# Performance work log

Measured on AMD Instinct MI355X. Metric: run time of the kernel, lower is better.

Reference implementation:

```python
import jax, jax.numpy as jnp
import numpy as np

B, S, D = 2, 1024, 1024
H, KVH, HD = 16, 4, 64  # query heads, kv heads, head_dim
EPS = 1e-5
SCALE = float(np.sqrt(HD))  # note: scale uses original head_dim, not concat dim


def rmsnorm(x, g):
    return x * jax.lax.rsqrt(jnp.mean(x * x, axis=-1, keepdims=True) + EPS) * g


def rope(x, cos, sin):
    # x: [B,S,h,HD]; cos/sin: [S, HD//2]; pairs are consecutive (view_as_complex layout)
    xr = x.reshape(*x.shape[:-1], HD // 2, 2)
    x0, x1 = xr[..., 0], xr[..., 1]
    c = cos[None, :, None, :]
    s = sin[None, :, None, :]
    o0 = x0 * c - x1 * s
    o1 = x0 * s + x1 * c
    return jnp.stack([o0, o1], axis=-1).reshape(x.shape)


def context_build(x, W, gq, gk):
    comb = x @ W.T  # [B,S, H*HD + 2*KVH*HD]
    q, k, v = jnp.split(comb, [H * HD, H * HD + KVH * HD], axis=-1)
    q = rmsnorm(q, gq).reshape(B, S, H, HD)
    k = rmsnorm(k, gk).reshape(B, S, KVH, HD)
    v = v.reshape(B, S, KVH, HD)
    return q, k, v


def setup_inputs() -> dict:
    key = jax.random.key(0)
    ks = jax.random.split(key, 12)
    total = H * HD + 2 * KVH * HD  # 1536
    pos = jnp.arange(S, dtype=jnp.float32)
    theta = 10000.0 ** (-jnp.arange(0, HD, 2, dtype=jnp.float32) / HD)  # [HD//2]
    ang = pos[:, None] * theta[None, :]  # [S, HD//2]
    sc = 0.02
    return {
        "local_c": jax.random.normal(ks[0], (B, S, D), jnp.float32),
        "global_c": jax.random.normal(ks[1], (B, S, D), jnp.float32),
        "freqs_cos": jnp.cos(ang),
        "freqs_sin": jnp.sin(ang),
        "W_lc": jax.random.normal(ks[2], (total, D), jnp.float32) * sc,
        "W_gc": jax.random.normal(ks[3], (total, D), jnp.float32) * sc,
        "g_q_lc": jnp.ones((H * HD,), jnp.float32),
        "g_k_lc": jnp.ones((KVH * HD,), jnp.float32),
        "g_q_gc": jnp.ones((H * HD,), jnp.float32),
        "g_k_gc": jnp.ones((KVH * HD,), jnp.float32),
        "W_local": jax.random.normal(ks[4], (H * HD, 2 * H * HD), jnp.float32) * sc,
        "b_local": jnp.zeros((H * HD,), jnp.float32),
        "g_lc_out": jnp.ones((H * HD,), jnp.float32),
        "W_global": jax.random.normal(ks[5], (H * HD, 2 * H * HD), jnp.float32) * sc,
        "b_global": jnp.zeros((H * HD,), jnp.float32),
        "g_gc_out": jnp.ones((H * HD,), jnp.float32),
    }


def reference(local_c, global_c, freqs_cos, freqs_sin, W_lc, W_gc,
              g_q_lc, g_k_lc, g_q_gc, g_k_gc,
              W_local, b_local, g_lc_out, W_global, b_global, g_gc_out):
    q_lc, k_lc, v_lc = context_build(local_c, W_lc, g_q_lc, g_k_lc)
    q_gc, k_gc, v_gc = context_build(global_c, W_gc, g_q_gc, g_k_gc)

    q_lc = rope(q_lc, freqs_cos, freqs_sin)
    k_lc = rope(k_lc, freqs_cos, freqs_sin)
    q_gc = rope(q_gc, freqs_cos, freqs_sin)
    k_gc = rope(k_gc, freqs_cos, freqs_sin)

    # concat local+global along head_dim -> per-head dim 2*HD
    q = jnp.concatenate([q_lc, q_gc], axis=-1)  # [B,S,H,2HD]
    k = jnp.concatenate([k_lc, k_gc], axis=-1)  # [B,S,KVH,2HD]
    v = jnp.concatenate([v_lc, v_gc], axis=-1)

    n_rep = H // KVH
    k = jnp.repeat(k, n_rep, axis=2)  # [B,S,H,2HD] (GQA repeat_kv)
    v = jnp.repeat(v, n_rep, axis=2)

    scores = jnp.einsum("bqhd,bkhd->bhqk", q, k) / SCALE  # [B,H,S,S]
    attn = jax.nn.softmax(scores, axis=-1)
    out = jnp.einsum("bhqk,bkhd->bqhd", attn, v).reshape(B, S, H * 2 * HD)

    x_lc = rmsnorm(out @ W_local.T + b_local, g_lc_out)
    x_gc = rmsnorm(out @ W_global.T + b_global, g_gc_out)
    return (x_lc, x_gc)
```

## Files before the change

kernel.cpp:

```cpp
#include <hip/hip_runtime.h>

typedef __attribute__((ext_vector_type(8))) __bf16 bf16x8;
typedef __attribute__((ext_vector_type(4))) __bf16 bf16x4;
typedef __attribute__((ext_vector_type(4))) float f32x4;

__device__ __forceinline__ bf16x8 cvt8(const float* __restrict__ p)
{
    const float4 a = *(const float4*)p;
    const float4 b = *(const float4*)(p + 4);
    bf16x8 r;
    r[0] = (__bf16)a.x; r[1] = (__bf16)a.y; r[2] = (__bf16)a.z; r[3] = (__bf16)a.w;
    r[4] = (__bf16)b.x; r[5] = (__bf16)b.y; r[6] = (__bf16)b.z; r[7] = (__bf16)b.w;
    return r;
}

__device__ __forceinline__ void gld16(const __bf16* g, __bf16* l)
{
    __builtin_amdgcn_global_load_lds(
        (const __attribute__((address_space(1))) void*)g,
        (__attribute__((address_space(3))) void*)l, 16, 0, 0);
}

struct CvtArgs {
    const float* s[6];
    __bf16* d[6];
    int n[6];
};

__global__ __launch_bounds__(256) void cvt_bf16(CvtArgs a)
{
    const int t = blockIdx.y;
    const int i0 = (blockIdx.x * 256 + threadIdx.x) * 8;
    if (i0 < a.n[t])
        *(bf16x8*)(a.d[t] + i0) = cvt8(a.s[t] + i0);
}

template <typename CT>
__device__ __forceinline__ void gemm_core(const __bf16* __restrict__ Ap, int lda,
                                          const __bf16* __restrict__ Bp, int ldb,
                                          CT* __restrict__ Cp, int ldc, int K)
{
    __shared__ __bf16 As[128 * 32];
    __shared__ __bf16 Bs[128 * 32];
    const int tid  = threadIdx.x;
    const int w    = tid >> 6;
    const int lane = tid & 63;
    const int ln   = lane & 15;
    const int quad = lane >> 4;
    const int wm   = w & 1;
    const int wn   = w >> 1;

    const int srow = 32 * w + (lane >> 2);
    const int scol = (lane & 3) * 8;

    f32x4 acc[4][4];
    const f32x4 zero = {0.f, 0.f, 0.f, 0.f};
#pragma unroll
    for (int i = 0; i < 4; i++)
#pragma unroll
        for (int j = 0; j < 4; j++) acc[i][j] = zero;

    for (int k0 = 0; k0 < K; k0 += 32) {
        __syncthreads();
        gld16(Ap + (size_t)srow * lda        + k0 + scol, As + (2 * w)     * 512 + lane * 8);
        gld16(Ap + (size_t)(srow + 16) * lda + k0 + scol, As + (2 * w + 1) * 512 + lane * 8);
        gld16(Bp + (size_t)srow * ldb        + k0 + scol, Bs + (2 * w)     * 512 + lane * 8);
        gld16(Bp + (size_t)(srow + 16) * ldb + k0 + scol, Bs + (2 * w + 1) * 512 + lane * 8);
        __syncthreads();

        bf16x8 af[4], bw[4];
#pragma unroll
        for (int i = 0; i < 4; i++)
            af[i] = *(const bf16x8*)(As + (wm * 64 + i * 16 + ln) * 32 + quad * 8);
#pragma unroll
        for (int j = 0; j < 4; j++)
            bw[j] = *(const bf16x8*)(Bs + (wn * 64 + j * 16 + ln) * 32 + quad * 8);
#pragma unroll
        for (int i = 0; i < 4; i++)
#pragma unroll
            for (int j = 0; j < 4; j++)
                acc[i][j] = __builtin_amdgcn_mfma_f32_16x16x32_bf16(
                    af[i], bw[j], acc[i][j], 0, 0, 0);
    }

#pragma unroll
    for (int i = 0; i < 4; i++)
#pragma unroll
        for (int j = 0; j < 4; j++)
#pragma unroll
            for (int r = 0; r < 4; r++) {
                const int ml = wm * 64 + i * 16 + quad * 4 + r;
                const int nl = wn * 64 + j * 16 + ln;
                Cp[(size_t)ml * ldc + nl] = (CT)acc[i][j][r];
            }
}

__global__ __launch_bounds__(256) void gemm_qkv(const __bf16* __restrict__ Xbf,
                                                const __bf16* __restrict__ Wqkv,
                                                __bf16* __restrict__ comb)
{
    const int z = blockIdx.z;
    const __bf16* A = Xbf  + (size_t)z * 2048 * 1024 + (size_t)blockIdx.y * 128 * 1024;
    const __bf16* B = Wqkv + (size_t)z * 1536 * 1024 + (size_t)blockIdx.x * 128 * 1024;
    __bf16* C = comb + (size_t)z * 2048 * 1536 +
                (size_t)blockIdx.y * 128 * 1536 + (size_t)blockIdx.x * 128;
    gemm_core<__bf16>(A, 1024, B, 1024, C, 1536, 1024);
}

__global__ __launch_bounds__(256) void gemm_out(const __bf16* __restrict__ AO,
                                                const __bf16* __restrict__ Wout,
                                                float* __restrict__ Y0,
                                                float* __restrict__ Y1)
{
    const int kh = blockIdx.z;
    const __bf16* A = AO   + (size_t)blockIdx.y * 128 * 2048 + kh * 1024;
    const __bf16* B = Wout + (size_t)blockIdx.x * 128 * 2048 + kh * 1024;
    float* Y = kh ? Y1 : Y0;
    float* C = Y + (size_t)blockIdx.y * 128 * 2048 + (size_t)blockIdx.x * 128;
    gemm_core<float>(A, 2048, B, 2048, C, 2048, 1024);
}

__global__ __launch_bounds__(256) void pack_qkv(
    const __bf16* __restrict__ comb,
    const float* __restrict__ fcos, const float* __restrict__ fsin,
    const float* __restrict__ g_q_lc, const float* __restrict__ g_k_lc,
    const float* __restrict__ g_q_gc, const float* __restrict__ g_k_gc,
    __bf16* __restrict__ Qb, __bf16* __restrict__ Kb, __bf16* __restrict__ Vtb)
{
    const int m = blockIdx.x, ctx = blockIdx.y;
    const int b = m >> 10, s = m & 1023;
    const int tid = threadIdx.x;
    const __bf16* cr = comb + ((size_t)ctx * 2048 + m) * 1536;
    const float* gq = ctx ? g_q_gc : g_q_lc;
    const float* gk = ctx ? g_k_gc : g_k_lc;

    const bf16x4 qv = *(const bf16x4*)(cr + tid * 4);
    float sq = (float)qv[0] * (float)qv[0] + (float)qv[1] * (float)qv[1] +
               (float)qv[2] * (float)qv[2] + (float)qv[3] * (float)qv[3];
    const float kvv = (float)cr[1024 + tid];
    float sk = kvv * kvv;
#pragma unroll
    for (int off = 32; off > 0; off >>= 1) {
        sq += __shfl_down(sq, off);
        sk += __shfl_down(sk, off);
    }
    __shared__ float redq[4], redk[4];
    if ((tid & 63) == 0) { redq[tid >> 6] = sq; redk[tid >> 6] = sk; }
    __syncthreads();
    sq = redq[0] + redq[1] + redq[2] + redq[3];
    sk = redk[0] + redk[1] + redk[2] + redk[3];
    const float rq = rsqrtf(sq * (1.f / 1024.f) + 1e-5f);
    const float rk = rsqrtf(sk * (1.f / 256.f) + 1e-5f);

#pragma unroll
    for (int pp = 0; pp < 2; pp++) {
        const int p = tid + pp * 256;
        const int h = p >> 5, pi = p & 31;
        const float x0 = (float)cr[2 * p]     * rq * gq[2 * p];
        const float x1 = (float)cr[2 * p + 1] * rq * gq[2 * p + 1];
        const float c  = fcos[s * 32 + pi];
        const float sn = fsin[s * 32 + pi];
        const float o0 = x0 * c - x1 * sn;
        const float o1 = x0 * sn + x1 * c;
        const size_t qo = ((size_t)m * 16 + h) * 128 + ctx * 64 + 2 * pi;
        Qb[qo]     = (__bf16)o0;
        Qb[qo + 1] = (__bf16)o1;
    }
    if (tid < 128) {
        const int p = tid;
        const int kvh = p >> 5, pi = p & 31;
        const float x0 = (float)cr[1024 + 2 * p]     * rk * gk[2 * p];
        const float x1 = (float)cr[1024 + 2 * p + 1] * rk * gk[2 * p + 1];
        const float c  = fcos[s * 32 + pi];
        const float sn = fsin[s * 32 + pi];
        const float o0 = x0 * c - x1 * sn;
        const float o1 = x0 * sn + x1 * c;
        const size_t ko = ((size_t)(b * 4 + kvh) * 1024 + s) * 128 + ctx * 64 + 2 * pi;
        Kb[ko]     = (__bf16)o0;
        Kb[ko + 1] = (__bf16)o1;
    }
    {
        const int kvh = tid >> 6, d = tid & 63;
        Vtb[((size_t)(b * 4 + kvh) * 128 + ctx * 64 + d) * 1024 + s] = cr[1280 + tid];
    }
}

__global__ __launch_bounds__(256) void attn(const __bf16* __restrict__ Qb,
                                            const __bf16* __restrict__ Kb,
                                            const __bf16* __restrict__ Vtb,
                                            __bf16* __restrict__ AO)
{
    __shared__ __bf16 Ks[64][136];
    __shared__ __bf16 Vts[128][72];
    __shared__ __bf16 Ps[4][16][72];

    const int tid  = threadIdx.x;
    const int w    = tid >> 6;
    const int lane = tid & 63;
    const int ln   = lane & 15;
    const int quad = lane >> 4;
    const int qt = blockIdx.x, h = blockIdx.y, b = blockIdx.z;
    const int kv = h >> 2;

    const __bf16* Kbase = Kb  + (size_t)(b * 4 + kv) * 1024 * 128;
    const __bf16* Vbase = Vtb + (size_t)(b * 4 + kv) * 128 * 1024;

    bf16x8 qf[4];
    const int qrow = qt * 64 + w * 16 + ln;
    const __bf16* qptr = Qb + ((size_t)(b * 1024 + qrow) * 16 + h) * 128;
#pragma unroll
    for (int kc = 0; kc < 4; kc++)
        qf[kc] = *(const bf16x8*)(qptr + kc * 32 + quad * 8);

    f32x4 oacc[8];
    const f32x4 zero = {0.f, 0.f, 0.f, 0.f};
#pragma unroll
    for (int j = 0; j < 8; j++) oacc[j] = zero;
    float mrow[4], lrow[4];
#pragma unroll
    for (int r = 0; r < 4; r++) { mrow[r] = -1e30f; lrow[r] = 0.f; }

    for (int kt = 0; kt < 16; kt++) {
        __syncthreads();
        const int ks0 = kt * 64;
#pragma unroll
        for (int c = tid; c < 1024; c += 256) {
            const int row = c >> 4, seg = c & 15;
            *(bf16x8*)&Ks[row][seg * 8] =
                *(const bf16x8*)(Kbase + (size_t)(ks0 + row) * 128 + seg * 8);
        }
#pragma unroll
        for (int c = tid; c < 1024; c += 256) {
            const int row = c >> 3, seg = c & 7;
            *(bf16x8*)&Vts[row][seg * 8] =
                *(const bf16x8*)(Vbase + (size_t)row * 1024 + ks0 + seg * 8);
        }
        __syncthreads();

        f32x4 sacc[4];
#pragma unroll
        for (int j = 0; j < 4; j++) {
            f32x4 a = zero;
#pragma unroll
            for (int kc = 0; kc < 4; kc++) {
                const bf16x8 kf =
                    *(const bf16x8*)&Ks[j * 16 + ln][kc * 32 + quad * 8];
                a = __builtin_amdgcn_mfma_f32_16x16x32_bf16(qf[kc], kf, a, 0, 0, 0);
            }
            sacc[j] = a * 0.125f;
        }

        float alpha_[4], pexp[4][4];
#pragma unroll
        for (int r = 0; r < 4; r++) {
            float mx = fmaxf(fmaxf(sacc[0][r], sacc[1][r]),
                             fmaxf(sacc[2][r], sacc[3][r]));
#pragma unroll
            for (int off = 1; off < 16; off <<= 1)
                mx = fmaxf(mx, __shfl_xor(mx, off));
            const float mn = fmaxf(mrow[r], mx);
            alpha_[r] = __expf(mrow[r] - mn);
            mrow[r] = mn;
            float rs = 0.f;
#pragma unroll
            for (int j = 0; j < 4; j++) {
                const float p = __expf(sacc[j][r] - mn);
                pexp[j][r] = p;
                rs += p;
            }
#pragma unroll
            for (int off = 1; off < 16; off <<= 1)
                rs += __shfl_xor(rs, off);
            lrow[r] = lrow[r] * alpha_[r] + rs;
        }
#pragma unroll
        for (int j2 = 0; j2 < 8; j2++) {
            f32x4 o = oacc[j2];
#pragma unroll
            for (int r = 0; r < 4; r++) o[r] *= alpha_[r];
            oacc[j2] = o;
        }
#pragma unroll
        for (int j = 0; j < 4; j++)
#pragma unroll
            for (int r = 0; r < 4; r++)
                Ps[w][quad * 4 + r][j * 16 + ln] = (__bf16)pexp[j][r];
        __syncthreads();
#pragma unroll
        for (int kk = 0; kk < 2; kk++) {
            const bf16x8 pf = *(const bf16x8*)&Ps[w][ln][kk * 32 + quad * 8];
#pragma unroll
            for (int j2 = 0; j2 < 8; j2++) {
                const bf16x8 vf =
                    *(const bf16x8*)&Vts[j2 * 16 + ln][kk * 32 + quad * 8];
                oacc[j2] = __builtin_amdgcn_mfma_f32_16x16x32_bf16(pf, vf, oacc[j2], 0, 0, 0);
            }
        }
    }

    float inv[4];
#pragma unroll
    for (int r = 0; r < 4; r++) inv[r] = 1.f / lrow[r];
#pragma unroll
    for (int j2 = 0; j2 < 8; j2++)
#pragma unroll
        for (int r = 0; r < 4; r++) {
            const size_t row = (size_t)(b * 1024 + qt * 64 + w * 16 + quad * 4 + r);
            AO[row * 2048 + h * 128 + j2 * 16 + ln] = (__bf16)(oacc[j2][r] * inv[r]);
        }
}

__global__ __launch_bounds__(256) void rmsnorm_out(const float* __restrict__ Y0,
                                                   const float* __restrict__ Y1,
                                                   const float* __restrict__ b_l,
                                                   const float* __restrict__ b_g,
                                                   const float* __restrict__ g_l,
                                                   const float* __restrict__ g_g,
                                                   float* __restrict__ out)
{
    const int m = blockIdx.x, which = blockIdx.y;
    const int tid = threadIdx.x;
    const size_t off = (size_t)m * 2048 + which * 1024 + tid * 4;
    const float* bias = which ? b_g : b_l;
    const float* g    = which ? g_g : g_l;

    const float4 y0 = *(const float4*)(Y0 + off);
    const float4 y1 = *(const float4*)(Y1 + off);
    const float4 bv = *(const float4*)(bias + tid * 4);
    float x[4];
    x[0] = y0.x + y1.x + bv.x;
    x[1] = y0.y + y1.y + bv.y;
    x[2] = y0.z + y1.z + bv.z;
    x[3] = y0.w + y1.w + bv.w;
    float ss = x[0] * x[0] + x[1] * x[1] + x[2] * x[2] + x[3] * x[3];
#pragma unroll
    for (int off2 = 32; off2 > 0; off2 >>= 1) ss += __shfl_down(ss, off2);
    __shared__ float red[4];
    if ((tid & 63) == 0) red[tid >> 6] = ss;
    __syncthreads();
    ss = red[0] + red[1] + red[2] + red[3];
    const float r = rsqrtf(ss * (1.f / 1024.f) + 1e-5f);

    const float4 gv = *(const float4*)(g + tid * 4);
    float4 o;
    o.x = x[0] * r * gv.x;
    o.y = x[1] * r * gv.y;
    o.z = x[2] * r * gv.z;
    o.w = x[3] * r * gv.w;
    *(float4*)(out + (size_t)which * 2097152 + (size_t)m * 1024 + tid * 4) = o;
}

extern "C" void kernel_launch(void* const* d_in, const int* in_sizes, int n_in,
                              void* d_out, int out_size, void* d_ws, size_t ws_size,
                              hipStream_t stream)
{
    (void)in_sizes; (void)n_in; (void)out_size; (void)ws_size;
    const float* local_c  = (const float*)d_in[0];
    const float* global_c = (const float*)d_in[1];
    const float* fcos     = (const float*)d_in[2];
    const float* fsin     = (const float*)d_in[3];
    const float* W_lc     = (const float*)d_in[4];
    const float* W_gc     = (const float*)d_in[5];
    const float* g_q_lc   = (const float*)d_in[6];
    const float* g_k_lc   = (const float*)d_in[7];
    const float* g_q_gc   = (const float*)d_in[8];
    const float* g_k_gc   = (const float*)d_in[9];
    const float* W_local  = (const float*)d_in[10];
    const float* b_local  = (const float*)d_in[11];
    const float* g_lc_out = (const float*)d_in[12];
    const float* W_global = (const float*)d_in[13];
    const float* b_global = (const float*)d_in[14];
    const float* g_gc_out = (const float*)d_in[15];

    char* ws = (char*)d_ws;
    __bf16* Wout = (__bf16*)(ws + 0);
    __bf16* Xbf  = (__bf16*)(ws + 8388608);
    __bf16* Wqkv = (__bf16*)(ws + 16777216);
    __bf16* comb = (__bf16*)(ws + 23068672);
    __bf16* Qb   = (__bf16*)(ws + 35651584);
    __bf16* Kb   = (__bf16*)(ws + 44040192);
    __bf16* Vtb  = (__bf16*)(ws + 46137344);
    __bf16* AO   = (__bf16*)(ws + 48234496);
    float*  Y0   = (float*)(ws + 8388608);
    float*  Y1   = (float*)(ws + 25165824);

    CvtArgs ca;
    ca.s[0] = local_c;  ca.d[0] = Xbf;            ca.n[0] = 2097152;
    ca.s[1] = global_c; ca.d[1] = Xbf + 2097152;  ca.n[1] = 2097152;
    ca.s[2] = W_lc;     ca.d[2] = Wqkv;           ca.n[2] = 1572864;
    ca.s[3] = W_gc;     ca.d[3] = Wqkv + 1572864; ca.n[3] = 1572864;
    ca.s[4] = W_local;  ca.d[4] = Wout;           ca.n[4] = 2097152;
    ca.s[5] = W_global; ca.d[5] = Wout + 2097152; ca.n[5] = 2097152;

    cvt_bf16<<<dim3(1024, 6), 256, 0, stream>>>(ca);
    gemm_qkv<<<dim3(12, 16, 2), 256, 0, stream>>>(Xbf, Wqkv, comb);
    pack_qkv<<<dim3(2048, 2), 256, 0, stream>>>(comb, fcos, fsin,
                                                g_q_lc, g_k_lc, g_q_gc, g_k_gc,
                                                Qb, Kb, Vtb);
    attn<<<dim3(16, 16, 2), 256, 0, stream>>>(Qb, Kb, Vtb, AO);
    gemm_out<<<dim3(16, 16, 2), 256, 0, stream>>>(AO, Wout, Y0, Y1);
    rmsnorm_out<<<dim3(2048, 2), 256, 0, stream>>>(Y0, Y1, b_local, b_global,
                                                   g_lc_out, g_gc_out,
                                                   (float*)d_out);
}
```

Measured before the change: 255.6 us.

## Double-buffer GEMM and attention tiles and fold softmax scale into Q

The GEMM core now uses two LDS buffers. It issues the async global-to-LDS loads for the next K slice before computing on the current one, which drops one barrier per step. The attention kernel prefetches the next K/V tile into registers while computing, writes it into a second LDS buffer at the end of the iteration, and drops the barrier between the per-wave P write and read. The 1/8 score scale moves into the Q RoPE epilogue (a power of two, so exact in bf16), removing a multiply per score. This costs double the LDS and extra registers, which may lower occupancy.

Result: faster. 235.9 us (-7.7%).

```diff
diff --git a/kernel.cpp b/kernel.cpp
--- a/kernel.cpp
+++ b/kernel.cpp
@@ -40,8 +40,8 @@
                                           const __bf16* __restrict__ Bp, int ldb,
                                           CT* __restrict__ Cp, int ldc, int K)
 {
-    __shared__ __bf16 As[128 * 32];
-    __shared__ __bf16 Bs[128 * 32];
+    __shared__ __bf16 As[2][128 * 32];
+    __shared__ __bf16 Bs[2][128 * 32];
     const int tid  = threadIdx.x;
     const int w    = tid >> 6;
     const int lane = tid & 63;
@@ -60,21 +60,26 @@
 #pragma unroll
         for (int j = 0; j < 4; j++) acc[i][j] = zero;
 
-    for (int k0 = 0; k0 < K; k0 += 32) {
+    auto stage = [&](int buf, int k0) {
+        gld16(Ap + (size_t)srow * lda        + k0 + scol, As[buf] + (2 * w)     * 512 + lane * 8);
+        gld16(Ap + (size_t)(srow + 16) * lda + k0 + scol, As[buf] + (2 * w + 1) * 512 + lane * 8);
+        gld16(Bp + (size_t)srow * ldb        + k0 + scol, Bs[buf] + (2 * w)     * 512 + lane * 8);
+        gld16(Bp + (size_t)(srow + 16) * ldb + k0 + scol, Bs[buf] + (2 * w + 1) * 512 + lane * 8);
+    };
+
+    stage(0, 0);
+    int buf = 0;
+    for (int k0 = 0; k0 < K; k0 += 32, buf ^= 1) {
         __syncthreads();
-        gld16(Ap + (size_t)srow * lda        + k0 + scol, As + (2 * w)     * 512 + lane * 8);
-        gld16(Ap + (size_t)(srow + 16) * lda + k0 + scol, As + (2 * w + 1) * 512 + lane * 8);
-        gld16(Bp + (size_t)srow * ldb        + k0 + scol, Bs + (2 * w)     * 512 + lane * 8);
-        gld16(Bp + (size_t)(srow + 16) * ldb + k0 + scol, Bs + (2 * w + 1) * 512 + lane * 8);
-        __syncthreads();
+        if (k0 + 32 < K) stage(buf ^ 1, k0 + 32);
 
         bf16x8 af[4], bw[4];
 #pragma unroll
         for (int i = 0; i < 4; i++)
-            af[i] = *(const bf16x8*)(As + (wm * 64 + i * 16 + ln) * 32 + quad * 8);
+            af[i] = *(const bf16x8*)(As[buf] + (wm * 64 + i * 16 + ln) * 32 + quad * 8);
 #pragma unroll
         for (int j = 0; j < 4; j++)
-            bw[j] = *(const bf16x8*)(Bs + (wn * 64 + j * 16 + ln) * 32 + quad * 8);
+            bw[j] = *(const bf16x8*)(Bs[buf] + (wn * 64 + j * 16 + ln) * 32 + quad * 8);
 #pragma unroll
         for (int i = 0; i < 4; i++)
 #pragma unroll
@@ -160,8 +165,8 @@
         const float x1 = (float)cr[2 * p + 1] * rq * gq[2 * p + 1];
         const float c  = fcos[s * 32 + pi];
         const float sn = fsin[s * 32 + pi];
-        const float o0 = x0 * c - x1 * sn;
-        const float o1 = x0 * sn + x1 * c;
+        const float o0 = (x0 * c - x1 * sn) * 0.125f;
+        const float o1 = (x0 * sn + x1 * c) * 0.125f;
         const size_t qo = ((size_t)m * 16 + h) * 128 + ctx * 64 + 2 * pi;
         Qb[qo]     = (__bf16)o0;
         Qb[qo + 1] = (__bf16)o1;
@@ -190,8 +195,8 @@
                                             const __bf16* __restrict__ Vtb,
                                             __bf16* __restrict__ AO)
 {
-    __shared__ __bf16 Ks[64][136];
-    __shared__ __bf16 Vts[128][72];
+    __shared__ __bf16 Ks[2][64][136];
+    __shared__ __bf16 Vts[2][128][72];
     __shared__ __bf16 Ps[4][16][72];
 
     const int tid  = threadIdx.x;
@@ -220,21 +225,31 @@
 #pragma unroll
     for (int r = 0; r < 4; r++) { mrow[r] = -1e30f; lrow[r] = 0.f; }
 
+    bf16x8 kreg[4], vreg[4];
+    auto load_tiles = [&](int kt) {
+        const int ks0 = kt * 64;
+#pragma unroll
+        for (int i = 0; i < 4; i++) {
+            const int c = tid + i * 256;
+            kreg[i] = *(const bf16x8*)(Kbase + (size_t)(ks0 + (c >> 4)) * 128 + (c & 15) * 8);
+            vreg[i] = *(const bf16x8*)(Vbase + (size_t)(c >> 3) * 1024 + ks0 + (c & 7) * 8);
+        }
+    };
+    auto write_tiles = [&](int buf) {
+#pragma unroll
+        for (int i = 0; i < 4; i++) {
+            const int c = tid + i * 256;
+            *(bf16x8*)&Ks[buf][c >> 4][(c & 15) * 8] = kreg[i];
+            *(bf16x8*)&Vts[buf][c >> 3][(c & 7) * 8] = vreg[i];
+        }
+    };
+
+    load_tiles(0);
+    write_tiles(0);
+
     for (int kt = 0; kt < 16; kt++) {
-        __syncthreads();
-        const int ks0 = kt * 64;
-#pragma unroll
-        for (int c = tid; c < 1024; c += 256) {
-            const int row = c >> 4, seg = c & 15;
-            *(bf16x8*)&Ks[row][seg * 8] =
-                *(const bf16x8*)(Kbase + (size_t)(ks0 + row) * 128 + seg * 8);
-        }
-#pragma unroll
-        for (int c = tid; c < 1024; c += 256) {
-            const int row = c >> 3, seg = c & 7;
-            *(bf16x8*)&Vts[row][seg * 8] =
-                *(const bf16x8*)(Vbase + (size_t)row * 1024 + ks0 + seg * 8);
-        }
+        const int buf = kt & 1;
+        if (kt + 1 < 16) load_tiles(kt + 1);
         __syncthreads();
 
         f32x4 sacc[4];
@@ -244,10 +259,10 @@
 #pragma unroll
             for (int kc = 0; kc < 4; kc++) {
                 const bf16x8 kf =
-                    *(const bf16x8*)&Ks[j * 16 + ln][kc * 32 + quad * 8];
+                    *(const bf16x8*)&Ks[buf][j * 16 + ln][kc * 32 + quad * 8];
                 a = __builtin_amdgcn_mfma_f32_16x16x32_bf16(qf[kc], kf, a, 0, 0, 0);
             }
-            sacc[j] = a * 0.125f;
+            sacc[j] = a;
         }
 
         float alpha_[4], pexp[4][4];
@@ -285,17 +300,18 @@
 #pragma unroll
             for (int r = 0; r < 4; r++)
                 Ps[w][quad * 4 + r][j * 16 + ln] = (__bf16)pexp[j][r];
-        __syncthreads();
 #pragma unroll
         for (int kk = 0; kk < 2; kk++) {
             const bf16x8 pf = *(const bf16x8*)&Ps[w][ln][kk * 32 + quad * 8];
 #pragma unroll
             for (int j2 = 0; j2 < 8; j2++) {
                 const bf16x8 vf =
-                    *(const bf16x8*)&Vts[j2 * 16 + ln][kk * 32 + quad * 8];
+                    *(const bf16x8*)&Vts[buf][j2 * 16 + ln][kk * 32 + quad * 8];
                 oacc[j2] = __builtin_amdgcn_mfma_f32_16x16x32_bf16(pf, vf, oacc[j2], 0, 0, 0);
             }
         }
+
+        if (kt + 1 < 16) write_tiles(buf ^ 1);
     }
 
     float inv[4];
```
